# Kernel optimization log

Measured on AMD Instinct MI355X. Metric: run time of the kernel, lower is better.

The kernel has to match this reference:

```python
import jax, jax.numpy as jnp
import numpy as np

C, H = 256, 256  # feat_num, feat_h (equirect is H x 2H)


def setup_inputs() -> dict:
    key = jax.random.key(0)
    ks = jax.random.split(key, 6)
    m = jax.random.normal(ks[0], (1, C, H, 2 * H), jnp.float32)
    b = jax.random.normal(ks[1], (1, C, H, H), jnp.float32)
    u = jax.random.normal(ks[2], (1, C, H, H), jnp.float32)
    d = jax.random.normal(ks[3], (1, C, H, H), jnp.float32)
    Wf = jax.random.normal(ks[4], (C, C, 3, 3), jnp.float32) * 0.02
    bf = jnp.zeros((C,), jnp.float32)
    Wm = jax.random.normal(ks[5], (1, 2 * C, 1, 1), jnp.float32) * 0.02
    bm = jnp.zeros((1,), jnp.float32)
    return {"m": m, "b": b, "u": u, "d": d, "Wf": Wf, "bf": bf, "Wm": Wm, "bm": bm}


def _cube2equi(cube, out_h, out_w):
    # cube: [6, C, h, h]; face order: 0 back(z-), 1 down(y-), 2 front(z+), 3 left(x-), 4 right(x+), 5 up(y+)
    h = cube.shape[-1]
    theta = (jnp.arange(out_w, dtype=cube.dtype) + 0.5) / out_w * (2.0 * jnp.pi) - jnp.pi  # longitude [-pi, pi)
    phi = jnp.pi / 2 - (jnp.arange(out_h, dtype=cube.dtype) + 0.5) / out_h * jnp.pi        # latitude [pi/2, -pi/2]
    st, ct = jnp.sin(theta)[None, :], jnp.cos(theta)[None, :]
    sp, cp = jnp.sin(phi)[:, None], jnp.cos(phi)[:, None]
    dx = cp * st
    dy = jnp.broadcast_to(sp, (out_h, out_w))
    dz = cp * ct
    ax, ay, az = jnp.abs(dx), jnp.abs(dy), jnp.abs(dz)
    mx = jnp.maximum(jnp.maximum(ax, ay), az)
    px, py, pz = dx / mx, dy / mx, dz / mx
    cond_z = (az >= ax) & (az >= ay)
    cond_x = (~cond_z) & (ax >= ay)
    face = jnp.where(cond_z, jnp.where(dz > 0, 2, 0),
           jnp.where(cond_x, jnp.where(dx > 0, 4, 3),
                              jnp.where(dy > 0, 5, 1)))
    a = jnp.where(cond_z, jnp.where(dz > 0, px, -px),
        jnp.where(cond_x, jnp.where(dx > 0, -pz, pz), px))
    bcoord = jnp.where(cond_z | cond_x, -py, jnp.where(dy > 0, pz, -pz))
    uu = jnp.clip((a + 1.0) * 0.5 * (h - 1), 0.0, h - 1)
    vv = jnp.clip((bcoord + 1.0) * 0.5 * (h - 1), 0.0, h - 1)
    u0 = jnp.floor(uu).astype(jnp.int32); v0 = jnp.floor(vv).astype(jnp.int32)
    u1 = jnp.minimum(u0 + 1, h - 1); v1 = jnp.minimum(v0 + 1, h - 1)
    wu = uu - u0; wv = vv - v0

    def samp(vi, ui):
        return cube[face, :, vi, ui]  # [out_h, out_w, C] gather over all channels

    out = (samp(v0, u0) * ((1 - wv) * (1 - wu))[..., None]
         + samp(v0, u1) * ((1 - wv) * wu)[..., None]
         + samp(v1, u0) * (wv * (1 - wu))[..., None]
         + samp(v1, u1) * (wv * wu)[..., None])
    return jnp.transpose(out, (2, 0, 1))  # [C, out_h, out_w]


def _conv(x, w, bias, pad):
    y = jax.lax.conv_general_dilated(x, w, (1, 1), [(pad, pad), (pad, pad)],
                                     dimension_numbers=("NCHW", "OIHW", "NCHW"))
    return y + bias[None, :, None, None]


def reference(m, b, u, d, Wf, bf, Wm, bm):
    h = b.shape[-1]
    empty = jnp.zeros_like(b[0])  # the torch module's zero 'emptyFace' parameter
    # faces stacked as [back, down, empty, empty, empty, up], vectorized over all channels
    cube = jnp.stack([b[0], d[0], empty, empty, empty, u[0]])  # [6, C, h, h]
    aux = _cube2equi(cube, h, 2 * h)[None]                      # [1, C, h, 2h]
    M_aux = jax.nn.relu(_conv(aux, Wf, bf, 1))
    M_main = jax.nn.relu(_conv(m, Wf, bf, 1))
    mask = jax.nn.sigmoid(_conv(jnp.concatenate([M_main, M_aux], axis=1), Wm, bm, 0))
    return m + mask * M_aux
```

## Files before the change

### kernel.cpp

```cpp
#include <hip/hip_runtime.h>
#include <hip/hip_bf16.h>

#define NPIX 131072
#define WP   514
#define XP_BYTES 67897344
#define XP_STRIDE 67962880
#define FT_BYTES 100663296

typedef __attribute__((ext_vector_type(8))) short bf16x8;
typedef __attribute__((ext_vector_type(4))) float f32x4;

typedef const __attribute__((address_space(1))) void g_cvoid;
typedef __attribute__((address_space(3))) void l_void;

__device__ __forceinline__ void async16(const void* g, void* l) {
  __builtin_amdgcn_global_load_lds((g_cvoid*)g, (l_void*)l, 16, 0, 0);
}

__global__ void zero_borders(__hip_bfloat16* Xm, __hip_bfloat16* Xa) {
  int i = blockIdx.x;
  __hip_bfloat16* X = blockIdx.y ? Xa : Xm;
  long ppix;
  if (i < 514)       ppix = i;
  else if (i < 1028) ppix = 257L * WP + (i - 514);
  else if (i < 1284) ppix = (long)(i - 1028 + 1) * WP;
  else               ppix = (long)(i - 1284 + 1) * WP + 513;
  ((unsigned int*)(X + ppix * 256))[threadIdx.x] = 0u;
}

__global__ void zero_mask(float* maskacc) {
  maskacc[blockIdx.x * 256 + threadIdx.x] = 0.f;
}

__global__ void prep_weights(const float* __restrict__ Wf, __hip_bfloat16* __restrict__ Wtt) {
  int idx = blockIdx.x * 256 + threadIdx.x;
  int cout = idx / 2304, rem = idx % 2304;
  int o = rem >> 8, ci = rem & 255;
  Wtt[(((o << 5) + (ci >> 3)) << 11) + (cout << 3) + (ci & 7)] =
      __float2bfloat16(Wf[(cout * 256 + ci) * 9 + o]);
}

__global__ void nchw_to_pad_nhwc(const float* __restrict__ src, __hip_bfloat16* __restrict__ Xp) {
  __shared__ __align__(16) __hip_bfloat16 tile[64 * 264];
  int tid = threadIdx.x;
  int p0 = blockIdx.x * 64;
  int cw = tid >> 4;
  int px4 = (tid & 15) << 2;
  for (int it = 0; it < 16; ++it) {
    int c = (it << 4) + cw;
    float4 v = *(const float4*)&src[(long)c * NPIX + p0 + px4];
    tile[(px4 + 0) * 264 + c] = __float2bfloat16(v.x);
    tile[(px4 + 1) * 264 + c] = __float2bfloat16(v.y);
    tile[(px4 + 2) * 264 + c] = __float2bfloat16(v.z);
    tile[(px4 + 3) * 264 + c] = __float2bfloat16(v.w);
  }
  __syncthreads();
  int y = p0 >> 9, x0 = p0 & 511;
  long basep = (long)(y + 1) * WP + x0 + 1;
  for (int pass = 0; pass < 8; ++pass) {
    int tpx = (pass << 3) + (tid >> 5);
    int chunk = tid & 31;
    uint4 v = *(const uint4*)&tile[tpx * 264 + (chunk << 3)];
    *(uint4*)&Xp[(basep + tpx) * 256 + (chunk << 3)] = v;
  }
}

__global__ void face_to_nhwc(const float* __restrict__ fb, const float* __restrict__ fd,
                             const float* __restrict__ fu, __hip_bfloat16* __restrict__ Ft) {
  __shared__ __align__(16) __hip_bfloat16 tile[64 * 264];
  int tid = threadIdx.x;
  int face = blockIdx.x >> 10;
  int p0 = (blockIdx.x & 1023) << 6;
  const float* src = (face == 0) ? fb : (face == 1) ? fd : fu;
  int cw = tid >> 4;
  int px4 = (tid & 15) << 2;
  for (int it = 0; it < 16; ++it) {
    int c = (it << 4) + cw;
    float4 v = *(const float4*)&src[(long)c * 65536 + p0 + px4];
    tile[(px4 + 0) * 264 + c] = __float2bfloat16(v.x);
    tile[(px4 + 1) * 264 + c] = __float2bfloat16(v.y);
    tile[(px4 + 2) * 264 + c] = __float2bfloat16(v.z);
    tile[(px4 + 3) * 264 + c] = __float2bfloat16(v.w);
  }
  __syncthreads();
  long basep = ((long)face << 16) + p0;
  for (int pass = 0; pass < 8; ++pass) {
    int tpx = (pass << 3) + (tid >> 5);
    int chunk = tid & 31;
    uint4 v = *(const uint4*)&tile[tpx * 264 + (chunk << 3)];
    *(uint4*)&Ft[((basep + tpx) << 8) + (chunk << 3)] = v;
  }
}

__device__ __forceinline__ void bf8_fma(uint4 q, float w, float* acc) {
  unsigned x;
  x = q.x; acc[0] += w * __uint_as_float(x << 16); acc[1] += w * __uint_as_float(x & 0xffff0000u);
  x = q.y; acc[2] += w * __uint_as_float(x << 16); acc[3] += w * __uint_as_float(x & 0xffff0000u);
  x = q.z; acc[4] += w * __uint_as_float(x << 16); acc[5] += w * __uint_as_float(x & 0xffff0000u);
  x = q.w; acc[6] += w * __uint_as_float(x << 16); acc[7] += w * __uint_as_float(x & 0xffff0000u);
}

__global__ void aux_gen_v2(const __hip_bfloat16* __restrict__ Ft,
                           __hip_bfloat16* __restrict__ Xp) {
  const int lane = threadIdx.x & 63;
  const int p = (blockIdx.x << 2) + (threadIdx.x >> 6);
  const int yy = p >> 9, xx = p & 511;

  float theta = ((xx + 0.5f) / 512.f) * 6.283185307179586f - 3.141592653589793f;
  float phi   = 1.5707963267948966f - ((yy + 0.5f) / 256.f) * 3.141592653589793f;
  float st = __sinf(theta), ct = __cosf(theta);
  float sp = __sinf(phi),   cp = __cosf(phi);
  float dx = cp * st, dy = sp, dz = cp * ct;
  float ax = fabsf(dx), ay = fabsf(dy), az = fabsf(dz);
  float mx = fmaxf(fmaxf(ax, ay), az);
  float pxn = dx / mx, pyn = dy / mx, pzn = dz / mx;
  bool cz = (az >= ax) && (az >= ay);
  bool cx = (!cz) && (ax >= ay);
  int face; float a, b;
  if (cz)      { face = dz > 0.f ? 2 : 0; a = dz > 0.f ? pxn : -pxn; b = -pyn; }
  else if (cx) { face = dx > 0.f ? 4 : 3; a = dx > 0.f ? -pzn : pzn; b = -pyn; }
  else         { face = dy > 0.f ? 5 : 1; a = pxn; b = dy > 0.f ? pzn : -pzn; }
  float uu = fminf(fmaxf((a + 1.f) * 0.5f * 255.f, 0.f), 255.f);
  float vv = fminf(fmaxf((b + 1.f) * 0.5f * 255.f, 0.f), 255.f);

  const long outbase = ((long)((yy + 1) * WP + xx + 1)) << 8;
  const int c0 = (lane >> 1) << 3;
  const int up = lane & 1;
  const int slot = (face == 0) ? 0 : (face == 1) ? 1 : (face == 5) ? 2 : -1;

  if (slot < 0) {
    if (!up) *(uint4*)&Xp[outbase + c0] = make_uint4(0u, 0u, 0u, 0u);
    return;
  }
  int u0 = (int)uu, v0 = (int)vv;
  int u1 = min(u0 + 1, 255), v1 = min(v0 + 1, 255);
  float wu = uu - (float)u0, wv = vv - (float)v0;
  int uc = up ? u1 : u0;
  float wA = up ? wu : (1.f - wu);
  const __hip_bfloat16* base = Ft + ((long)slot << 24);

  float acc[8] = {0.f, 0.f, 0.f, 0.f, 0.f, 0.f, 0.f, 0.f};
  uint4 q0 = *(const uint4*)&base[(((long)(v0 << 8) + uc) << 8) + c0];
  uint4 q1 = *(const uint4*)&base[(((long)(v1 << 8) + uc) << 8) + c0];
  bf8_fma(q0, (1.f - wv) * wA, acc);
  bf8_fma(q1, wv * wA, acc);
#pragma unroll
  for (int j = 0; j < 8; ++j) acc[j] += __shfl_xor(acc[j], 1);
  if (!up) {
    union { uint4 q; __hip_bfloat16 h[8]; } o;
#pragma unroll
    for (int j = 0; j < 8; ++j) o.h[j] = __float2bfloat16(acc[j]);
    *(uint4*)&Xp[outbase + c0] = o.q;
  }
}

__global__ void aux_gen(const float* __restrict__ fb, const float* __restrict__ fd,
                        const float* __restrict__ fu,
                        __hip_bfloat16* __restrict__ Xp) {
  __shared__ __align__(16) __hip_bfloat16 tile[64 * 264];
  int tid = threadIdx.x;
  int p0 = blockIdx.x * 64;
  int px = tid & 63, w = tid >> 6;

  int p = p0 + px;
  int yy = p >> 9, xx = p & 511;
  float theta = ((xx + 0.5f) / 512.f) * 6.283185307179586f - 3.141592653589793f;
  float phi   = 1.5707963267948966f - ((yy + 0.5f) / 256.f) * 3.141592653589793f;
  float st = __sinf(theta), ct = __cosf(theta);
  float sp = __sinf(phi),   cp = __cosf(phi);
  float dx = cp * st, dy = sp, dz = cp * ct;
  float ax = fabsf(dx), ay = fabsf(dy), az = fabsf(dz);
  float mx = fmaxf(fmaxf(ax, ay), az);
  float pxn = dx / mx, pyn = dy / mx, pzn = dz / mx;
  bool cz = (az >= ax) && (az >= ay);
  bool cx = (!cz) && (ax >= ay);
  int face; float a, b;
  if (cz)      { face = dz > 0.f ? 2 : 0; a = dz > 0.f ? pxn : -pxn; b = -pyn; }
  else if (cx) { face = dx > 0.f ? 4 : 3; a = dx > 0.f ? -pzn : pzn; b = -pyn; }
  else         { face = dy > 0.f ? 5 : 1; a = pxn; b = dy > 0.f ? pzn : -pzn; }
  float uu = fminf(fmaxf((a + 1.f) * 0.5f * 255.f, 0.f), 255.f);
  float vv = fminf(fmaxf((b + 1.f) * 0.5f * 255.f, 0.f), 255.f);

  const float* F = (face == 0) ? fb : (face == 1) ? fd : (face == 5) ? fu : nullptr;
  int u0 = (int)uu, v0 = (int)vv;
  int u1 = min(u0 + 1, 255), v1 = min(v0 + 1, 255);
  float wu = uu - (float)u0, wv = vv - (float)v0;
  float w00 = (1.f - wv) * (1.f - wu), w01 = (1.f - wv) * wu;
  float w10 = wv * (1.f - wu),         w11 = wv * wu;
  int i00 = v0 * 256 + u0, i01 = v0 * 256 + u1;
  int i10 = v1 * 256 + u0, i11 = v1 * 256 + u1;
  for (int k = 0; k < 64; ++k) {
    int c = (k << 2) + w;
    float val = 0.f;
    if (F) {
      const float* Fc = F + ((long)c << 16);
      val = w00 * Fc[i00] + w01 * Fc[i01] + w10 * Fc[i10] + w11 * Fc[i11];
    }
    tile[px * 264 + c] = __float2bfloat16(val);
  }
  __syncthreads();
  int y = p0 >> 9, x0g = p0 & 511;
  long basep = (long)(y + 1) * WP + x0g + 1;
  for (int pass = 0; pass < 8; ++pass) {
    int tpx = (pass << 3) + (tid >> 5);
    int chunk = tid & 31;
    uint4 v = *(const uint4*)&tile[tpx * 264 + (chunk << 3)];
    *(uint4*)&Xp[(basep + tpx) * 256 + (chunk << 3)] = v;
  }
}

__global__ __launch_bounds__(512, 4)
void conv3x3_mfma(const __hip_bfloat16* __restrict__ Xpa,
                  const __hip_bfloat16* __restrict__ Xpm,
                  const __hip_bfloat16* __restrict__ Wtt,
                  const float* __restrict__ bias,
                  const float* __restrict__ wm,
                  __hip_bfloat16* __restrict__ Out,
                  float* __restrict__ maskacc) {
  __shared__ __align__(16) __hip_bfloat16 At[4 * 80 * 32];
  const int tid = threadIdx.x;
  const int wave = tid >> 6, lane = tid & 63;
  const bool aux = (blockIdx.y == 0);
  const __hip_bfloat16* __restrict__ Xp = aux ? Xpa : Xpm;
  const float* __restrict__ wmv = aux ? wm + 256 : wm;

  const int tile = ((blockIdx.x & 7) << 7) + (blockIdx.x >> 3);
  const int x0 = (tile >> 7) << 6;
  const int y0 = (tile & 127) << 1;
  const int wrow = wave >> 2;
  const int n_off = (wave & 3) << 6;
  const int lq = lane >> 4, ln = lane & 15;

  const int srow = wave >> 1;
  const long stage_row = (long)(y0 + srow) * WP + x0;
  const int s_col = lane >> 2;
  const int s_ci  = (lane & 3) << 3;

  f32x4 acc[4][4] = {};

  for (int s = 0; s < 8; ++s) {
    const int ci0 = s << 5;
    if (wave & 1) {
      async16(Xp + ((stage_row + 48 + s_col) << 8) + ci0 + s_ci, &At[(srow * 80 + 48) << 5]);
      async16(Xp + ((stage_row + 64 + s_col) << 8) + ci0 + s_ci, &At[(srow * 80 + 64) << 5]);
    } else {
      async16(Xp + ((stage_row +  0 + s_col) << 8) + ci0 + s_ci, &At[(srow * 80 +  0) << 5]);
      async16(Xp + ((stage_row + 16 + s_col) << 8) + ci0 + s_ci, &At[(srow * 80 + 16) << 5]);
      async16(Xp + ((stage_row + 32 + s_col) << 8) + ci0 + s_ci, &At[(srow * 80 + 32) << 5]);
    }
    __syncthreads();
#pragma unroll
    for (int o = 0; o < 9; ++o) {
      const int dy = o / 3, dxo = o % 3;
      const int arow = (wrow + dy) * 80;
      bf16x8 af[4], bb[4];
#pragma unroll
      for (int mi = 0; mi < 4; ++mi)
        af[mi] = *(const bf16x8*)&At[((arow + mi * 16 + ln + dxo) << 5) + (lq << 3)];
#pragma unroll
      for (int ni = 0; ni < 4; ++ni)
        bb[ni] = *(const bf16x8*)&Wtt[(((o << 5) + (s << 2) + lq) << 11) +
                                      ((n_off + ni * 16 + ln) << 3)];
#pragma unroll
      for (int mi = 0; mi < 4; ++mi)
#pragma unroll
        for (int ni = 0; ni < 4; ++ni)
          acc[mi][ni] = __builtin_amdgcn_mfma_f32_16x16x32_bf16(af[mi], bb[ni], acc[mi][ni], 0, 0, 0);
    }
    __syncthreads();
  }

  float bv[4], wv[4];
#pragma unroll
  for (int ni = 0; ni < 4; ++ni) {
    int cc = n_off + ni * 16 + ln;
    bv[ni] = bias[cc];
    wv[ni] = wmv[cc];
  }
  const int prow = (y0 + wrow) * 512 + x0;
#pragma unroll
  for (int mi = 0; mi < 4; ++mi) {
#pragma unroll
    for (int r = 0; r < 4; ++r) {
      int pix = prow + mi * 16 + (lq << 2) + r;
      float mp = 0.f;
#pragma unroll
      for (int ni = 0; ni < 4; ++ni) {
        float v = acc[mi][ni][r] + bv[ni];
        v = v > 0.f ? v : 0.f;
        if (aux) Out[((long)pix << 8) + (n_off + ni * 16 + ln)] = __float2bfloat16(v);
        mp += v * wv[ni];
      }
      mp += __shfl_xor(mp, 1);
      mp += __shfl_xor(mp, 2);
      mp += __shfl_xor(mp, 4);
      mp += __shfl_xor(mp, 8);
      if (ln == 0) atomicAdd(&maskacc[pix], mp);
    }
  }
}

__global__ void final_combine(const float* __restrict__ m,
                              const __hip_bfloat16* __restrict__ MauxT,
                              const float* __restrict__ maskacc,
                              const float* __restrict__ bm,
                              float* __restrict__ out) {
  __shared__ __align__(16) __hip_bfloat16 tile[64 * 264];
  __shared__ float sm[64];
  int tid = threadIdx.x;
  int p0 = blockIdx.x * 64;
  if (tid < 64) {
    float v = maskacc[p0 + tid] + bm[0];
    sm[tid] = 1.f / (1.f + expf(-v));
  }
#pragma unroll
  for (int j = 0; j < 8; ++j) {
    int f = j * 256 + tid;
    int px = f >> 5, c8 = f & 31;
    *(uint4*)&tile[px * 264 + (c8 << 3)] =
        *(const uint4*)&MauxT[(((long)(p0 + px)) << 8) + (c8 << 3)];
  }
  __syncthreads();
  int cw = tid >> 4;
  int px4 = (tid & 15) << 2;
  for (int it = 0; it < 16; ++it) {
    int c = (it << 4) + cw;
    long gi = (long)c * NPIX + p0 + px4;
    float4 mv = *(const float4*)&m[gi];
    float4 o;
    o.x = mv.x + sm[px4 + 0] * __bfloat162float(tile[(px4 + 0) * 264 + c]);
    o.y = mv.y + sm[px4 + 1] * __bfloat162float(tile[(px4 + 1) * 264 + c]);
    o.z = mv.z + sm[px4 + 2] * __bfloat162float(tile[(px4 + 2) * 264 + c]);
    o.w = mv.w + sm[px4 + 3] * __bfloat162float(tile[(px4 + 3) * 264 + c]);
    *(float4*)&out[gi] = o;
  }
}

extern "C" void kernel_launch(void* const* d_in, const int* in_sizes, int n_in,
                              void* d_out, int out_size, void* d_ws, size_t ws_size,
                              hipStream_t stream) {
  const float* m  = (const float*)d_in[0];
  const float* fb = (const float*)d_in[1];
  const float* fu = (const float*)d_in[2];
  const float* fd = (const float*)d_in[3];
  const float* Wf = (const float*)d_in[4];
  const float* bf = (const float*)d_in[5];
  const float* Wm = (const float*)d_in[6];
  const float* bm = (const float*)d_in[7];
  float* out = (float*)d_out;

  char* ws = (char*)d_ws;
  const size_t NEED_FAST = (size_t)FT_BYTES + XP_STRIDE + 1179648 + 67108864 + 524288;

  if (ws_size >= NEED_FAST) {
    __hip_bfloat16* Ft     = (__hip_bfloat16*)(ws);
    __hip_bfloat16* Xp_m   = (__hip_bfloat16*)(ws);
    __hip_bfloat16* Xp_aux = (__hip_bfloat16*)(ws + (size_t)FT_BYTES);
    __hip_bfloat16* Wtt    = (__hip_bfloat16*)(ws + (size_t)FT_BYTES + XP_STRIDE);
    __hip_bfloat16* MauxT  = (__hip_bfloat16*)(ws + (size_t)FT_BYTES + XP_STRIDE + 1179648);
    float* maskacc         = (float*)(ws + (size_t)FT_BYTES + XP_STRIDE + 1179648 + 67108864);

    face_to_nhwc<<<3072, 256, 0, stream>>>(fb, fd, fu, Ft);
    aux_gen_v2<<<32768, 256, 0, stream>>>(Ft, Xp_aux);
    nchw_to_pad_nhwc<<<2048, 256, 0, stream>>>(m, Xp_m);
    zero_borders<<<dim3(1540, 2), 128, 0, stream>>>(Xp_m, Xp_aux);
    prep_weights<<<2304, 256, 0, stream>>>(Wf, Wtt);
    zero_mask<<<512, 256, 0, stream>>>(maskacc);
    conv3x3_mfma<<<dim3(1024, 2), 512, 0, stream>>>(Xp_aux, Xp_m, Wtt, bf, Wm, MauxT, maskacc);
    final_combine<<<2048, 256, 0, stream>>>(m, MauxT, maskacc, bm, out);
  } else {
    __hip_bfloat16* Xp_m   = (__hip_bfloat16*)(ws);
    __hip_bfloat16* Xp_aux = (__hip_bfloat16*)(ws + (size_t)XP_STRIDE);
    __hip_bfloat16* Wtt    = (__hip_bfloat16*)(ws + 2uL * XP_STRIDE);
    __hip_bfloat16* MauxT  = (__hip_bfloat16*)(ws + 2uL * XP_STRIDE + 1179648);
    float* maskacc         = (float*)(ws + 2uL * XP_STRIDE + 1179648 + 67108864);

    zero_borders<<<dim3(1540, 2), 128, 0, stream>>>(Xp_m, Xp_aux);
    zero_mask<<<512, 256, 0, stream>>>(maskacc);
    prep_weights<<<2304, 256, 0, stream>>>(Wf, Wtt);
    nchw_to_pad_nhwc<<<2048, 256, 0, stream>>>(m, Xp_m);
    aux_gen<<<2048, 256, 0, stream>>>(fb, fd, fu, Xp_aux);
    conv3x3_mfma<<<dim3(1024, 2), 512, 0, stream>>>(Xp_aux, Xp_m, Wtt, bf, Wm, MauxT, maskacc);
    final_combine<<<2048, 256, 0, stream>>>(m, MauxT, maskacc, bm, out);
  }
}
```

Baseline: 741.4 us.

## Double channel chunk per LDS stage and XOR-swizzle LDS layout in conv

Each stage of the 3x3 conv MFMA kernel now loads 64 input channels instead of 32, which halves the number of stage iterations and the __syncthreads barriers. The LDS tile doubles in size. An XOR swizzle on the 16-byte channel chunks is added to both the async loads and the fragment reads to avoid LDS bank conflicts. The larger LDS footprint may lower occupancy, and the inner kk loop is kept rolled.

```diff
diff --git a/kernel.cpp b/kernel.cpp
--- a/kernel.cpp
+++ b/kernel.cpp
@@ -217,7 +217,7 @@
                   const float* __restrict__ wm,
                   __hip_bfloat16* __restrict__ Out,
                   float* __restrict__ maskacc) {
-  __shared__ __align__(16) __hip_bfloat16 At[4 * 80 * 32];
+  __shared__ __align__(16) __hip_bfloat16 At[4 * 80 * 64];
   const int tid = threadIdx.x;
   const int wave = tid >> 6, lane = tid & 63;
   const bool aux = (blockIdx.y == 0);
@@ -233,39 +233,44 @@
 
   const int srow = wave >> 1;
   const long stage_row = (long)(y0 + srow) * WP + x0;
-  const int s_col = lane >> 2;
-  const int s_ci  = (lane & 3) << 3;
+  const int q_px = lane >> 3;
+  const int q_ci = ((lane & 7) ^ q_px) << 3;
 
   f32x4 acc[4][4] = {};
 
-  for (int s = 0; s < 8; ++s) {
-    const int ci0 = s << 5;
-    if (wave & 1) {
-      async16(Xp + ((stage_row + 48 + s_col) << 8) + ci0 + s_ci, &At[(srow * 80 + 48) << 5]);
-      async16(Xp + ((stage_row + 64 + s_col) << 8) + ci0 + s_ci, &At[(srow * 80 + 64) << 5]);
-    } else {
-      async16(Xp + ((stage_row +  0 + s_col) << 8) + ci0 + s_ci, &At[(srow * 80 +  0) << 5]);
-      async16(Xp + ((stage_row + 16 + s_col) << 8) + ci0 + s_ci, &At[(srow * 80 + 16) << 5]);
-      async16(Xp + ((stage_row + 32 + s_col) << 8) + ci0 + s_ci, &At[(srow * 80 + 32) << 5]);
+  for (int s = 0; s < 4; ++s) {
+    const int ci0 = s << 6;
+#pragma unroll
+    for (int j = 0; j < 5; ++j) {
+      const int chunk = ((wave & 1) ? 40 : 0) + (j << 3);
+      async16(Xp + ((stage_row + chunk + q_px) << 8) + ci0 + q_ci,
+              &At[(srow * 80 + chunk) << 6]);
     }
     __syncthreads();
 #pragma unroll
     for (int o = 0; o < 9; ++o) {
       const int dy = o / 3, dxo = o % 3;
       const int arow = (wrow + dy) * 80;
-      bf16x8 af[4], bb[4];
-#pragma unroll
-      for (int mi = 0; mi < 4; ++mi)
-        af[mi] = *(const bf16x8*)&At[((arow + mi * 16 + ln + dxo) << 5) + (lq << 3)];
-#pragma unroll
-      for (int ni = 0; ni < 4; ++ni)
-        bb[ni] = *(const bf16x8*)&Wtt[(((o << 5) + (s << 2) + lq) << 11) +
-                                      ((n_off + ni * 16 + ln) << 3)];
-#pragma unroll
-      for (int mi = 0; mi < 4; ++mi)
+      const int sw = (ln + dxo) & 7;
+#pragma unroll 1
+      for (int kk = 0; kk < 2; ++kk) {
+        bf16x8 af[4], bb[4];
+#pragma unroll
+        for (int mi = 0; mi < 4; ++mi) {
+          const int px = arow + mi * 16 + ln + dxo;
+          af[mi] = *(const bf16x8*)&At[(px << 6) + ((((kk << 2) | lq) ^ sw) << 3)];
+        }
 #pragma unroll
         for (int ni = 0; ni < 4; ++ni)
-          acc[mi][ni] = __builtin_amdgcn_mfma_f32_16x16x32_bf16(af[mi], bb[ni], acc[mi][ni], 0, 0, 0);
+          bb[ni] = *(const bf16x8*)&Wtt[(((o << 5) + (s << 3) + (kk << 2) + lq) << 11) +
+                                        ((n_off + ni * 16 + ln) << 3)];
+#pragma unroll
+        for (int mi = 0; mi < 4; ++mi)
+#pragma unroll
+          for (int ni = 0; ni < 4; ++ni)
+            acc[mi][ni] = __builtin_amdgcn_mfma_f32_16x16x32_bf16(af[mi], bb[ni],
+                                                                  acc[mi][ni], 0, 0, 0);
+      }
     }
     __syncthreads();
   }
```

Measured after the change: 737.6 us. About the same (-0.5%).
